# Performance work log

Hardware: AMD Instinct MI355X
Metric: run time of the kernel (lower is better)

The kernel has to match this reference:

```python
import jax, jax.numpy as jnp
import numpy as np

EMBD_DIM = 1024
NUM_HEADS = 16
HEAD_DIM = EMBD_DIM // NUM_HEADS


def setup_inputs() -> dict:
    key = jax.random.key(0)
    ks = jax.random.split(key, 9)
    B, S, D = 2, 2048, EMBD_DIM
    scale = 1.0 / np.sqrt(D)
    return {
        "x": jax.random.normal(ks[0], (B, S, D), dtype=jnp.float32),
        "wq": jax.random.normal(ks[1], (D, D), dtype=jnp.float32) * scale,
        "bq": jnp.zeros((D,), dtype=jnp.float32),
        "wk": jax.random.normal(ks[2], (D, D), dtype=jnp.float32) * scale,
        "bk": jnp.zeros((D,), dtype=jnp.float32),
        "wv": jax.random.normal(ks[3], (D, D), dtype=jnp.float32) * scale,
        "bv": jnp.zeros((D,), dtype=jnp.float32),
        "wo": jax.random.normal(ks[4], (D, D), dtype=jnp.float32) * scale,
        "bo": jnp.zeros((D,), dtype=jnp.float32),
    }


def reference(x, wq, bq, wk, bk, wv, bv, wo, bo):
    B, S, D = x.shape
    H, hd = NUM_HEADS, HEAD_DIM
    # projections: weights stored as (in, out) so y = x @ w + b
    q = (x @ wq + bq).reshape(B, S, H, hd).transpose(0, 2, 1, 3)  # [B,H,S,hd]
    k = (x @ wk + bk).reshape(B, S, H, hd).transpose(0, 2, 1, 3)
    v = (x @ wv + bv).reshape(B, S, H, hd).transpose(0, 2, 1, 3)
    scores = jnp.einsum("bhqd,bhkd->bhqk", q, k) / jnp.sqrt(jnp.float32(hd))
    causal = jnp.tril(jnp.ones((S, S), dtype=bool))  # [S,S]
    neg = jnp.finfo(scores.dtype).min
    scores = jnp.where(causal[None, None, :, :], scores, neg)
    attn = jax.nn.softmax(scores, axis=-1)
    out = jnp.einsum("bhqk,bhkd->bhqd", attn, v)  # [B,H,S,hd]
    out = out.transpose(0, 2, 1, 3).reshape(B, S, D)
    return out @ wo + bo
```

## Files before the change

kernel.cpp:

```cpp
#include <hip/hip_runtime.h>
#include <math.h>

#define S_LEN 2048
#define BATCH 2
#define DMODEL 1024
#define NHEADS 16
#define MROWS 4096

typedef short bf8 __attribute__((ext_vector_type(8)));
typedef short bf4 __attribute__((ext_vector_type(4)));
typedef float f32x4 __attribute__((ext_vector_type(4)));
typedef unsigned short u16;

static __device__ inline u16 f2bf(float f) {
    union { float f; unsigned u; } v; v.f = f;
    unsigned r = v.u + 0x7fffu + ((v.u >> 16) & 1u);
    return (u16)(r >> 16);
}

static __device__ inline void load16(const void* g, void* l) {
    __builtin_amdgcn_global_load_lds(
        (const __attribute__((address_space(1))) unsigned int*)g,
        (__attribute__((address_space(3))) unsigned int*)l, 16, 0, 0);
}

__global__ __launch_bounds__(256) void prep_kernel(
    const float* __restrict__ x, u16* __restrict__ xb,
    const float* __restrict__ W0, const float* __restrict__ W1,
    const float* __restrict__ W2, const float* __restrict__ W3,
    u16* __restrict__ wT) {
    const int bx = blockIdx.x, t = threadIdx.x;
    if (bx < 2048) {
        int i = bx * 256 + t;
        const float4* p = (const float4*)x + (size_t)i * 2;
        float4 a = p[0], b = p[1];
        u16 tmp[8] = {f2bf(a.x), f2bf(a.y), f2bf(a.z), f2bf(a.w),
                      f2bf(b.x), f2bf(b.y), f2bf(b.z), f2bf(b.w)};
        ((uint4*)xb)[i] = *(uint4*)tmp;
        return;
    }
    __shared__ u16 Ls[64][65];
    const int id = bx - 2048;
    const int z = id >> 8, rem = id & 255;
    const int n0 = (rem & 15) * 64, k0 = (rem >> 4) * 64;
    const float* W = z == 0 ? W0 : z == 1 ? W1 : z == 2 ? W2 : W3;
    u16* Wt = wT + (size_t)z * 1024 * 1024;
    const int r = t >> 2, c4 = (t & 3) * 16;
    const float* p = W + (size_t)(k0 + r) * 1024 + n0 + c4;
#pragma unroll
    for (int i = 0; i < 16; i += 4) {
        float4 v = *(const float4*)(p + i);
        Ls[r][c4 + i + 0] = f2bf(v.x);
        Ls[r][c4 + i + 1] = f2bf(v.y);
        Ls[r][c4 + i + 2] = f2bf(v.z);
        Ls[r][c4 + i + 3] = f2bf(v.w);
    }
    __syncthreads();
    u16 tmp[16];
#pragma unroll
    for (int i = 0; i < 16; i++) tmp[i] = Ls[c4 + i][r];
    uint4* q = (uint4*)(Wt + (size_t)(n0 + r) * 1024 + k0 + c4);
    q[0] = *(uint4*)tmp;
    q[1] = *(uint4*)(tmp + 8);
}

template <int MODE>
__global__ __launch_bounds__(256) void gemm_mfma(
    const u16* __restrict__ A, const u16* __restrict__ Bt,
    const float* __restrict__ bqp, const float* __restrict__ bkp,
    const float* __restrict__ bvp,
    u16* __restrict__ qout, u16* __restrict__ kout, u16* __restrict__ vtout,
    float* __restrict__ fout, float qscale) {
    __shared__ __align__(16) u16 As[2][64 * 64];
    __shared__ __align__(16) u16 Bs[2][128 * 64];

    const int t = threadIdx.x, lane = t & 63, w = t >> 6;
    const int quad = lane >> 4, l16 = lane & 15;
    const int row0 = blockIdx.y * 64, col0 = blockIdx.x * 128;
    const int K = DMODEL;

    const int lrow = lane >> 3;
    const int koff = ((lane & 7) ^ lrow) * 8;
    const u16* ag = A + (size_t)(row0 + w * 16 + lrow) * K + koff;
    const u16* bg = Bt + (size_t)(col0 + w * 32 + lrow) * K + koff;
    const int swz = l16 & 7;

    f32x4 acc[2][4] = {};

    {
        u16* lA = As[0] + (w * 16) * 64;
        u16* lB = Bs[0] + (w * 32) * 64;
        load16(ag, lA);
        load16(ag + (size_t)8 * K, lA + 512);
#pragma unroll
        for (int d = 0; d < 4; d++)
            load16(bg + (size_t)d * 8 * K, lB + d * 512);
    }

#pragma unroll 2
    for (int it = 0; it < 16; it++) {
        const int buf = it & 1;
        __syncthreads();
        if (it + 1 < 16) {
            const int k0 = (it + 1) * 64;
            u16* lA = As[buf ^ 1] + (w * 16) * 64;
            u16* lB = Bs[buf ^ 1] + (w * 32) * 64;
            load16(ag + k0, lA);
            load16(ag + (size_t)8 * K + k0, lA + 512);
#pragma unroll
            for (int d = 0; d < 4; d++)
                load16(bg + (size_t)d * 8 * K + k0, lB + d * 512);
        }
#pragma unroll
        for (int kc = 0; kc < 2; kc++) {
            bf8 xf[4], wf[2];
#pragma unroll
            for (int ni = 0; ni < 4; ni++)
                xf[ni] = *(const bf8*)&As[buf][(ni * 16 + l16) * 64 +
                                              ((kc * 4 + quad) ^ swz) * 8];
#pragma unroll
            for (int mi = 0; mi < 2; mi++)
                wf[mi] = *(const bf8*)&Bs[buf][(w * 32 + mi * 16 + l16) * 64 +
                                              ((kc * 4 + quad) ^ swz) * 8];
#pragma unroll
            for (int mi = 0; mi < 2; mi++)
#pragma unroll
                for (int ni = 0; ni < 4; ni++)
                    acc[mi][ni] = __builtin_amdgcn_mfma_f32_16x16x32_bf16(
                        wf[mi], xf[ni], acc[mi][ni], 0, 0, 0);
        }
    }

    const int sect = (col0 + w * 32) >> 10;
#pragma unroll
    for (int mi = 0; mi < 2; mi++) {
        const int featb = col0 + w * 32 + mi * 16 + quad * 4;
        float b4[4];
#pragma unroll
        for (int reg = 0; reg < 4; reg++)
            b4[reg] = (MODE == 1 ? bqp : (sect == 0 ? bqp : sect == 1 ? bkp : bvp))
                          [(featb + reg) & 1023];
#pragma unroll
        for (int ni = 0; ni < 4; ni++) {
            const int xrow = row0 + ni * 16 + l16;
            if (MODE == 1) {
                float4 o;
                o.x = acc[mi][ni][0] + b4[0];
                o.y = acc[mi][ni][1] + b4[1];
                o.z = acc[mi][ni][2] + b4[2];
                o.w = acc[mi][ni][3] + b4[3];
                *(float4*)(fout + (size_t)xrow * 1024 + featb) = o;
            } else {
                const int cf = featb & 1023;
                if (sect == 0) {
                    u16 t4[4];
#pragma unroll
                    for (int reg = 0; reg < 4; reg++)
                        t4[reg] = f2bf((acc[mi][ni][reg] + b4[reg]) * qscale);
                    *(uint2*)(qout + (size_t)xrow * 1024 + cf) = *(uint2*)t4;
                } else if (sect == 1) {
                    u16 t4[4];
#pragma unroll
                    for (int reg = 0; reg < 4; reg++)
                        t4[reg] = f2bf(acc[mi][ni][reg] + b4[reg]);
                    *(uint2*)(kout + (size_t)xrow * 1024 + cf) = *(uint2*)t4;
                } else {
#pragma unroll
                    for (int reg = 0; reg < 4; reg++)
                        vtout[((size_t)(xrow >> 11) * 1024 + cf + reg) * S_LEN +
                              (xrow & 2047)] = f2bf(acc[mi][ni][reg] + b4[reg]);
                }
            }
        }
    }
}

__global__ __launch_bounds__(256) void attn_kernel(const u16* __restrict__ Qg,
                                                   const u16* __restrict__ Kg,
                                                   const u16* __restrict__ Vt,
                                                   u16* __restrict__ Og) {
    __shared__ __align__(16) u16 Ks[2][64][32];
    __shared__ __align__(16) u16 Vs[2][64][32];

    const int t = threadIdx.x, lane = t & 63, w = t >> 6;
    const int quad = lane >> 4, l16 = lane & 15;
    const int qt = 31 - blockIdx.y;
    const int bh = blockIdx.x, b = bh >> 4, h = bh & 15;
    const size_t base = (size_t)b * S_LEN * DMODEL + h * 64;
    const size_t vbase = ((size_t)b * 1024 + h * 64) * S_LEN;
    const int sr = t >> 2, sc = (t & 3) * 16;
    const int pl = sc >> 5;
    const int g0 = (sc >> 3) & 3;
    const int ss = (sr >> 1) & 3;
    const int swz = (l16 >> 1) & 3;

    const u16* kp = Kg + base + (size_t)sr * DMODEL + sc;
    const u16* vp = Vt + vbase + (size_t)sr * S_LEN + sc;
    uint4 k0r = *(const uint4*)kp, k1r = *(const uint4*)(kp + 8);
    uint4 v0r = *(const uint4*)vp, v1r = *(const uint4*)(vp + 8);

    const int niter = qt + 1;
    const int q0 = qt * 64;

    bf8 aq[2];
#pragma unroll
    for (int c = 0; c < 2; c++)
        aq[c] = *(const bf8*)(Qg + base +
            (size_t)(q0 + w * 16 + l16) * DMODEL + c * 32 + quad * 8);

    float lsum = 0.f;
    f32x4 oT[4] = {};

    for (int kt = 0; kt < niter; kt++) {
        __syncthreads();
        *(uint4*)&Ks[pl][sr][(g0 ^ ss) * 8] = k0r;
        *(uint4*)&Ks[pl][sr][((g0 + 1) ^ ss) * 8] = k1r;
        *(uint4*)&Vs[pl][sr][(g0 ^ ss) * 8] = v0r;
        *(uint4*)&Vs[pl][sr][((g0 + 1) ^ ss) * 8] = v1r;
        __syncthreads();
        if (kt + 1 < niter) {
            size_t ok = (size_t)(kt + 1) * 64 * DMODEL;
            int ov = (kt + 1) * 64;
            k0r = *(const uint4*)(kp + ok); k1r = *(const uint4*)(kp + ok + 8);
            v0r = *(const uint4*)(vp + ov); v1r = *(const uint4*)(vp + ov + 8);
        }

        f32x4 scv[4] = {};
        __builtin_amdgcn_s_setprio(1);
#pragma unroll
        for (int c = 0; c < 2; c++)
#pragma unroll
            for (int ns = 0; ns < 4; ns++) {
                bf8 ak = *(const bf8*)&Ks[c][ns * 16 + l16][(quad ^ swz) * 8];
                scv[ns] = __builtin_amdgcn_mfma_f32_16x16x32_bf16(
                    ak, aq[c], scv[ns], 0, 0, 0);
            }
        __builtin_amdgcn_s_setprio(0);

        const bool diag = (kt == qt);
        const int ql = w * 16 + l16;
#pragma unroll
        for (int ns = 0; ns < 4; ns++) {
            float p[4];
#pragma unroll
            for (int r = 0; r < 4; r++) {
                int key = ns * 16 + quad * 4 + r;
                p[r] = (diag && key > ql) ? 0.f
                                          : __builtin_amdgcn_exp2f(scv[ns][r]);
                lsum += p[r];
            }
            union { unsigned u[2]; bf4 v; } pk;
            pk.u[0] = (__float_as_uint(p[0]) >> 16) |
                      (__float_as_uint(p[1]) & 0xffff0000u);
            pk.u[1] = (__float_as_uint(p[2]) >> 16) |
                      (__float_as_uint(p[3]) & 0xffff0000u);
            __builtin_amdgcn_s_setprio(1);
#pragma unroll
            for (int ds = 0; ds < 4; ds++) {
                bf4 av = *(const bf4*)&Vs[ns >> 1][ds * 16 + l16]
                    [((((ns & 1) * 2 + (quad >> 1)) ^ swz) * 8) + (quad & 1) * 4];
                oT[ds] = __builtin_amdgcn_mfma_f32_16x16x16bf16_1k(
                    av, pk.v, oT[ds], 0, 0, 0);
            }
            __builtin_amdgcn_s_setprio(0);
        }
    }

    float l = lsum;
    l += __shfl_xor(l, 16, 64);
    l += __shfl_xor(l, 32, 64);
    const float inv = 1.f / l;
    const int qq = q0 + w * 16 + l16;
#pragma unroll
    for (int ds = 0; ds < 4; ds++) {
        u16 t4[4];
#pragma unroll
        for (int r = 0; r < 4; r++) t4[r] = f2bf(oT[ds][r] * inv);
        *(uint2*)(Og + base + (size_t)qq * DMODEL + ds * 16 + quad * 4) =
            *(uint2*)t4;
    }
}

extern "C" void kernel_launch(void* const* d_in, const int* in_sizes, int n_in,
                              void* d_out, int out_size, void* d_ws, size_t ws_size,
                              hipStream_t stream) {
    const float* x  = (const float*)d_in[0];
    const float* wq = (const float*)d_in[1];
    const float* bq = (const float*)d_in[2];
    const float* wk = (const float*)d_in[3];
    const float* bk = (const float*)d_in[4];
    const float* wv = (const float*)d_in[5];
    const float* bv = (const float*)d_in[6];
    const float* wo = (const float*)d_in[7];
    const float* bo = (const float*)d_in[8];
    float* out = (float*)d_out;

    const size_t E = (size_t)MROWS * DMODEL;
    u16* xb  = (u16*)d_out;
    u16* vt  = xb + E;
    u16* wT  = (u16*)d_ws;
    u16* woT = wT + 3145728;
    u16* qb  = wT + 4194304;
    u16* kb  = qb + E;
    u16* ob  = kb + E;

    dim3 blk(256);
    prep_kernel<<<3072, blk, 0, stream>>>(x, xb, wq, wk, wv, wo, wT);

    gemm_mfma<0><<<dim3(24, 64), blk, 0, stream>>>(
        xb, wT, bq, bk, bv, qb, kb, vt, nullptr, 0.18033688011112042f);

    dim3 agrid(BATCH * NHEADS, 32);
    attn_kernel<<<agrid, blk, 0, stream>>>(qb, kb, vt, ob);

    gemm_mfma<1><<<dim3(8, 64), blk, 0, stream>>>(
        ob, woT, bo, nullptr, nullptr, nullptr, nullptr, nullptr, out, 1.0f);
}
```

Baseline: 192.8 us.

## Enlarge GEMM tile to 128x128 with 2x2 warp grid, drop LDS double buffering

The projection GEMMs now use 128x128 block tiles with each wave computing a 64x64 sub-tile (4x4 MFMA accumulators) instead of 64x128 tiles with 32x64 per wave. This raises arithmetic intensity per LDS read and halves the grid. In exchange the double-buffered LDS prefetch is replaced by single-buffered load-sync-compute, so global loads no longer overlap with MFMA work. Register use also grows, which may lower occupancy.

Measured after the change: 191.5 us. No clear change (-0.7%).

```diff
diff --git a/kernel.cpp b/kernel.cpp
--- a/kernel.cpp
+++ b/kernel.cpp
@@ -71,59 +71,48 @@
     const float* __restrict__ bvp,
     u16* __restrict__ qout, u16* __restrict__ kout, u16* __restrict__ vtout,
     float* __restrict__ fout, float qscale) {
-    __shared__ __align__(16) u16 As[2][64 * 64];
-    __shared__ __align__(16) u16 Bs[2][128 * 64];
+    __shared__ __align__(16) u16 As[128 * 64];
+    __shared__ __align__(16) u16 Bs[128 * 64];
 
     const int t = threadIdx.x, lane = t & 63, w = t >> 6;
     const int quad = lane >> 4, l16 = lane & 15;
-    const int row0 = blockIdx.y * 64, col0 = blockIdx.x * 128;
+    const int wr = w >> 1, wc = w & 1;
+    const int row0 = blockIdx.y * 128, col0 = blockIdx.x * 128;
     const int K = DMODEL;
 
-    const int lrow = lane >> 3;
-    const int koff = ((lane & 7) ^ lrow) * 8;
-    const u16* ag = A + (size_t)(row0 + w * 16 + lrow) * K + koff;
-    const u16* bg = Bt + (size_t)(col0 + w * 32 + lrow) * K + koff;
+    const int srow = t >> 3;
+    const int ksw = ((t & 7) ^ (srow & 7)) * 8;
+    const u16* ag = A + (size_t)(row0 + srow) * K + ksw;
+    const u16* bg = Bt + (size_t)(col0 + srow) * K + ksw;
     const int swz = l16 & 7;
 
-    f32x4 acc[2][4] = {};
-
-    {
-        u16* lA = As[0] + (w * 16) * 64;
-        u16* lB = Bs[0] + (w * 32) * 64;
-        load16(ag, lA);
-        load16(ag + (size_t)8 * K, lA + 512);
-#pragma unroll
-        for (int d = 0; d < 4; d++)
-            load16(bg + (size_t)d * 8 * K, lB + d * 512);
-    }
-
-#pragma unroll 2
-    for (int it = 0; it < 16; it++) {
-        const int buf = it & 1;
+    f32x4 acc[4][4] = {};
+
+    u16* lA = As + (size_t)(w * 8) * 64;
+    u16* lB = Bs + (size_t)(w * 8) * 64;
+
+    for (int it = 0; it < 16; ++it) {
+        if (it) __syncthreads();
+        const int k0 = it * 64;
+#pragma unroll
+        for (int i = 0; i < 4; i++) {
+            load16(ag + (size_t)i * 32 * K + k0, lA + i * 32 * 64);
+            load16(bg + (size_t)i * 32 * K + k0, lB + i * 32 * 64);
+        }
         __syncthreads();
-        if (it + 1 < 16) {
-            const int k0 = (it + 1) * 64;
-            u16* lA = As[buf ^ 1] + (w * 16) * 64;
-            u16* lB = Bs[buf ^ 1] + (w * 32) * 64;
-            load16(ag + k0, lA);
-            load16(ag + (size_t)8 * K + k0, lA + 512);
-#pragma unroll
-            for (int d = 0; d < 4; d++)
-                load16(bg + (size_t)d * 8 * K + k0, lB + d * 512);
-        }
 #pragma unroll
         for (int kc = 0; kc < 2; kc++) {
-            bf8 xf[4], wf[2];
+            bf8 xf[4], wf[4];
 #pragma unroll
             for (int ni = 0; ni < 4; ni++)
-                xf[ni] = *(const bf8*)&As[buf][(ni * 16 + l16) * 64 +
-                                              ((kc * 4 + quad) ^ swz) * 8];
-#pragma unroll
-            for (int mi = 0; mi < 2; mi++)
-                wf[mi] = *(const bf8*)&Bs[buf][(w * 32 + mi * 16 + l16) * 64 +
-                                              ((kc * 4 + quad) ^ swz) * 8];
-#pragma unroll
-            for (int mi = 0; mi < 2; mi++)
+                xf[ni] = *(const bf8*)&As[(wr * 64 + ni * 16 + l16) * 64 +
+                                          ((kc * 4 + quad) ^ swz) * 8];
+#pragma unroll
+            for (int mi = 0; mi < 4; mi++)
+                wf[mi] = *(const bf8*)&Bs[(wc * 64 + mi * 16 + l16) * 64 +
+                                          ((kc * 4 + quad) ^ swz) * 8];
+#pragma unroll
+            for (int mi = 0; mi < 4; mi++)
 #pragma unroll
                 for (int ni = 0; ni < 4; ni++)
                     acc[mi][ni] = __builtin_amdgcn_mfma_f32_16x16x32_bf16(
@@ -131,10 +120,10 @@
         }
     }
 
-    const int sect = (col0 + w * 32) >> 10;
-#pragma unroll
-    for (int mi = 0; mi < 2; mi++) {
-        const int featb = col0 + w * 32 + mi * 16 + quad * 4;
+    const int sect = (col0 + wc * 64) >> 10;
+#pragma unroll
+    for (int mi = 0; mi < 4; mi++) {
+        const int featb = col0 + wc * 64 + mi * 16 + quad * 4;
         float b4[4];
 #pragma unroll
         for (int reg = 0; reg < 4; reg++)
@@ -142,7 +131,7 @@
                           [(featb + reg) & 1023];
 #pragma unroll
         for (int ni = 0; ni < 4; ni++) {
-            const int xrow = row0 + ni * 16 + l16;
+            const int xrow = row0 + wr * 64 + ni * 16 + l16;
             if (MODE == 1) {
                 float4 o;
                 o.x = acc[mi][ni][0] + b4[0];
@@ -307,12 +296,12 @@
     dim3 blk(256);
     prep_kernel<<<3072, blk, 0, stream>>>(x, xb, wq, wk, wv, wo, wT);
 
-    gemm_mfma<0><<<dim3(24, 64), blk, 0, stream>>>(
+    gemm_mfma<0><<<dim3(24, 32), blk, 0, stream>>>(
         xb, wT, bq, bk, bv, qb, kb, vt, nullptr, 0.18033688011112042f);
 
     dim3 agrid(BATCH * NHEADS, 32);
     attn_kernel<<<agrid, blk, 0, stream>>>(qb, kb, vt, ob);
 
-    gemm_mfma<1><<<dim3(8, 64), blk, 0, stream>>>(
+    gemm_mfma<1><<<dim3(8, 32), blk, 0, stream>>>(
         ob, woT, bo, nullptr, nullptr, nullptr, nullptr, nullptr, out, 1.0f);
 }
```
